# Kernel tuning notes

Measured on AMD Instinct MI355X. Metric: run time of the kernel, lower is better.

The kernel has to match this reference:

```python
import jax, jax.numpy as jnp
import numpy as np

D_MODEL = 1024
D_FFN = 4096
NUM_EXPERTS = 8
TOP_K = 2
EPS = 1e-7


def setup_inputs() -> dict:
    key = jax.random.key(0)
    ks = jax.random.split(key, 10)
    B, T = 2, 2048
    s = 0.02
    return {
        "x": jax.random.normal(ks[0], (B, T, D_MODEL), dtype=jnp.float32),
        "padding_mask": jnp.ones((B, T), dtype=bool),
        "rms_w": jnp.ones((D_MODEL,), dtype=jnp.float32),
        "router_w": jax.random.normal(ks[1], (NUM_EXPERTS, D_MODEL), dtype=jnp.float32) * s,
        "router_b": jnp.zeros((NUM_EXPERTS,), dtype=jnp.float32),
        "W1": jax.random.normal(ks[2], (NUM_EXPERTS, D_MODEL, D_FFN), dtype=jnp.float32) * s,
        "b1": jnp.zeros((NUM_EXPERTS, D_FFN), dtype=jnp.float32),
        "W2": jax.random.normal(ks[3], (NUM_EXPERTS, D_FFN, D_MODEL), dtype=jnp.float32) * s,
        "b2": jnp.zeros((NUM_EXPERTS, D_MODEL), dtype=jnp.float32),
        "W3": jax.random.normal(ks[4], (NUM_EXPERTS, D_MODEL, D_FFN), dtype=jnp.float32) * s,
        "b3": jnp.zeros((NUM_EXPERTS, D_FFN), dtype=jnp.float32),
    }


def reference(x, padding_mask, rms_w, router_w, router_b, W1, b1, W2, b2, W3, b3):
    B, T, d = x.shape
    # RMSNorm
    rms = jnp.sqrt(jnp.mean(x * x, axis=-1, keepdims=True) + EPS)
    xn = rms_w * (x / rms)
    xf = xn.reshape(-1, d)  # [N, d]

    # Router: softmax -> top-k -> renormalize
    logits = xf @ router_w.T + router_b            # [N, E]
    probs = jax.nn.softmax(logits, axis=-1)
    topv, topi = jax.lax.top_k(probs, TOP_K)       # [N, K]
    w = topv / jnp.sum(topv, axis=-1, keepdims=True)
    # Dense combine weights per (token, expert): sum of top-k weights routed to e
    combine = jnp.sum(jax.nn.one_hot(topi, NUM_EXPERTS, dtype=xf.dtype) * w[..., None], axis=1)  # [N, E]

    # Loop over experts via scan (one full-token SwiGLU FFN per expert, masked combine)
    def step(acc, params):
        W1e, b1e, W2e, b2e, W3e, b3e, ce = params
        h = jax.nn.silu(xf @ W1e + b1e) * (xf @ W3e + b3e)  # [N, d_ffn]
        y = h @ W2e + b2e                                    # [N, d]
        return acc + ce[:, None] * y, None

    out, _ = jax.lax.scan(step, jnp.zeros_like(xf), (W1, b1, W2, b2, W3, b3, combine.T))
    aux_loss = jnp.asarray(0.0, dtype=x.dtype)  # use_aux_loss only active in training mode
    return out.reshape(B, T, d), aux_loss
```

## Files before the change

### kernel.cpp

```cpp
#include <hip/hip_runtime.h>
#include <stdint.h>


#define NTOK 4096
#define DM   1024
#define DF   4096
#define NE   8
#define BM   128
#define MAX_RB 72
#define SLOT_CAP (MAX_RB * BM)

typedef _Float16 f16;
typedef __attribute__((ext_vector_type(8))) _Float16 f16x8;
typedef __attribute__((ext_vector_type(4))) _Float16 f16x4;
typedef __attribute__((ext_vector_type(4))) float    f32x4;
typedef __attribute__((ext_vector_type(2))) float    f32x2;

__device__ __forceinline__ void gl2lds16(const void* g, void* l) {
  __builtin_amdgcn_global_load_lds(
      (const __attribute__((address_space(1))) unsigned int*)g,
      (__attribute__((address_space(3))) unsigned int*)l, 16, 0, 0);
}

__global__ __launch_bounds__(256) void k_rms_router(
    const float* __restrict__ x, const float* __restrict__ rms_w,
    const float* __restrict__ rw, const float* __restrict__ rbias,
    f16* __restrict__ xn, int* __restrict__ topi, float* __restrict__ topw,
    int* __restrict__ counts)
{
  int t = blockIdx.x;
  int tid = threadIdx.x;
  const float* xr = x + (size_t)t * DM;
  f32x4 xv = *(const f32x4*)(xr + tid * 4);
  f32x4 gw = *(const f32x4*)(rms_w + tid * 4);
  f32x4 gv = xv * gw;

  float v[9];
  v[8] = xv[0]*xv[0] + xv[1]*xv[1] + xv[2]*xv[2] + xv[3]*xv[3];
#pragma unroll
  for (int e = 0; e < NE; ++e) {
    f32x4 wv = *(const f32x4*)(rw + e * DM + tid * 4);
    v[e] = gv[0]*wv[0] + gv[1]*wv[1] + gv[2]*wv[2] + gv[3]*wv[3];
  }
#pragma unroll
  for (int off = 32; off; off >>= 1) {
#pragma unroll
    for (int j = 0; j < 9; ++j) v[j] += __shfl_xor(v[j], off);
  }
  __shared__ float red[4][9];
  int wave = tid >> 6, lane = tid & 63;
  if (lane == 0) {
#pragma unroll
    for (int j = 0; j < 9; ++j) red[wave][j] = v[j];
  }
  __syncthreads();
  float tot[9];
#pragma unroll
  for (int j = 0; j < 9; ++j)
    tot[j] = red[0][j] + red[1][j] + red[2][j] + red[3][j];

  float rinv = 1.0f / sqrtf(tot[8] * (1.0f / DM) + 1e-7f);
  float lg[NE];
#pragma unroll
  for (int e = 0; e < NE; ++e) lg[e] = tot[e] * rinv + rbias[e];

  int e1 = 0; float b1v = lg[0];
#pragma unroll
  for (int e = 1; e < NE; ++e) if (lg[e] > b1v) { b1v = lg[e]; e1 = e; }
  int e2 = -1; float b2v = -1e30f;
#pragma unroll
  for (int e = 0; e < NE; ++e) if (e != e1 && lg[e] > b2v) { b2v = lg[e]; e2 = e; }

  float r2 = expf(b2v - b1v);
  float w1 = 1.0f / (1.0f + r2);
  float w2 = r2 * w1;

  if (tid == 0) {
    topi[t * 2 + 0] = e1; topi[t * 2 + 1] = e2;
    topw[t * 2 + 0] = w1; topw[t * 2 + 1] = w2;
    atomicAdd(&counts[e1], 1);
    atomicAdd(&counts[e2], 1);
  }
  f16x4 o;
#pragma unroll
  for (int i = 0; i < 4; ++i) o[i] = (f16)(gv[i] * rinv);
  *(f16x4*)(xn + (size_t)t * DM + tid * 4) = o;
}

__global__ void k_build(const int* __restrict__ counts, int* __restrict__ po,
                        int2* __restrict__ rbtable, int* __restrict__ total_rb)
{
  if (threadIdx.x != 0 || blockIdx.x != 0) return;
  int off = 0, idx = 0;
  for (int e = 0; e < NE; ++e) {
    int c = counts[e];
    po[e] = off;
    int nrb = (c + BM - 1) / BM;
    for (int r = 0; r < nrb; ++r) { rbtable[idx] = make_int2(e, off + r * BM); ++idx; }
    off += nrb * BM;
  }
  *total_rb = idx;
}

__global__ __launch_bounds__(256) void k_assign(
    const int* __restrict__ topi, const float* __restrict__ topw,
    const int* __restrict__ po, int* __restrict__ cursors,
    int* __restrict__ slot_token, float* __restrict__ slot_w)
{
  int t = blockIdx.x * 256 + threadIdx.x;
  if (t >= NTOK) return;
#pragma unroll
  for (int k = 0; k < 2; ++k) {
    int e = topi[t * 2 + k];
    int pos = atomicAdd(&cursors[e], 1);
    int slot = po[e] + pos;
    slot_token[slot] = t;
    slot_w[slot] = topw[t * 2 + k];
  }
}

__global__ __launch_bounds__(256) void k_convw(
    const float* __restrict__ W1, const float* __restrict__ W3,
    const float* __restrict__ W2, f16* __restrict__ w16)
{
  __shared__ f16 T[64][132];
  int g = blockIdx.x;
  int tensor = g >> 12;
  int rem = g & 4095;
  int e = rem >> 9;
  int t = rem & 511;
  const float* W; int nstride, np, kt;
  if (tensor == 2) { W = W2; nstride = DM; np = t >> 6; kt = t & 63; }
  else { W = (tensor == 0) ? W1 : W3; nstride = DF; np = t >> 4; kt = t & 15; }
  const float* src = W + (size_t)e * DM * DF + (size_t)(kt * 64) * nstride + np * 128;

  int tid = threadIdx.x;
  int q = tid & 31, kb = tid >> 5;
#pragma unroll
  for (int i = 0; i < 8; ++i) {
    int k = kb + 8 * i;
    f32x4 v = *(const f32x4*)(src + (size_t)k * nstride + q * 4);
    f16x4 h4 = { (f16)v[0], (f16)v[1], (f16)v[2], (f16)v[3] };
    *(f16x4*)(&T[k][q * 4]) = h4;
  }
  __syncthreads();
  int n = tid >> 1;
  f16* dst = w16 + ((size_t)(tensor * NE + e) * 512 + t) * 8192 + n * 64 + (tid & 1) * 32;
#pragma unroll
  for (int qq = 0; qq < 4; ++qq) {
    int cs = (tid & 1) * 4 + qq;
    int cl = cs ^ (n & 7);
    f16x8 o;
#pragma unroll
    for (int j = 0; j < 8; ++j) o[j] = T[cl * 8 + j][n];
    *(f16x8*)(dst + qq * 8) = o;
  }
}

__global__ __launch_bounds__(256, 2) void k_ffn13(
    const f16* __restrict__ xn, const int* __restrict__ slot_token,
    const int2* __restrict__ rbtable, const int* __restrict__ total_rb,
    const f16* __restrict__ w16,
    const float* __restrict__ b1, const float* __restrict__ b3,
    f16* __restrict__ h)
{
  int bid = blockIdx.x;
  int wl = (bid & 7) * 288 + (bid >> 3);
  int rbi = wl % 72;
  int np  = wl / 72;
  if (rbi >= *total_rb) return;
  int2 ent = rbtable[rbi];
  int e = ent.x, row0 = ent.y;
  int n0 = np * 128;

  __shared__ __align__(16) f16 As[128 * 64];
  __shared__ __align__(16) f16 Bs[2][128 * 64];

  int tid = threadIdx.x, lane = tid & 63, wave = tid >> 6;
  int wm = wave >> 1, wn = wave & 1;

  const f16* wb1 = w16 + ((size_t)(0 * NE + e) * 512 + np * 16) * 8192;
  const f16* wb3 = w16 + ((size_t)(1 * NE + e) * 512 + np * 16) * 8192;

  int tok[4];
#pragma unroll
  for (int q = 0; q < 4; ++q) {
    int m = q * 32 + wave * 8 + (lane >> 3);
    int tkn = slot_token[row0 + m];
    tok[q] = (tkn < 0) ? 0 : tkn;
  }
  int csx = (((lane & 7) ^ (lane >> 3)) << 3);
  int lin = wave * 512 + lane * 8;

  f32x4 acc1[4][4], acc3[4][4];
  f32x4 z = {0.f, 0.f, 0.f, 0.f};
#pragma unroll
  for (int i = 0; i < 4; ++i)
#pragma unroll
    for (int j = 0; j < 4; ++j) { acc1[i][j] = z; acc3[i][j] = z; }

  for (int kt = 0; kt < DM / 64; ++kt) {
    int k0 = kt * 64;
    const f16* s1 = wb1 + (size_t)kt * 8192;
    const f16* s3 = wb3 + (size_t)kt * 8192;
#pragma unroll
    for (int q = 0; q < 4; ++q) {
      gl2lds16(xn + (size_t)tok[q] * DM + k0 + csx,
               (char*)As + q * 4096 + wave * 1024);
      gl2lds16(s1 + q * 2048 + lin, (char*)Bs[0] + q * 4096 + wave * 1024);
      gl2lds16(s3 + q * 2048 + lin, (char*)Bs[1] + q * 4096 + wave * 1024);
    }
    __syncthreads();
#pragma unroll
    for (int kh = 0; kh < 2; ++kh) {
      int kk = kh * 32 + (lane >> 4) * 8;
      f16x8 a[4];
#pragma unroll
      for (int fm = 0; fm < 4; ++fm) {
        int m = wm * 64 + fm * 16 + (lane & 15);
        a[fm] = *(const f16x8*)((char*)As + m * 128 + 2 * (kk ^ ((m & 7) << 3)));
      }
#pragma unroll
      for (int fn = 0; fn < 4; ++fn) {
        int n = wn * 64 + fn * 16 + (lane & 15);
        f16x8 bf1 = *(const f16x8*)((char*)Bs[0] + n * 128 + 2 * (kk ^ ((n & 7) << 3)));
        f16x8 bf3 = *(const f16x8*)((char*)Bs[1] + n * 128 + 2 * (kk ^ ((n & 7) << 3)));
#pragma unroll
        for (int fm = 0; fm < 4; ++fm) {
          acc1[fm][fn] = __builtin_amdgcn_mfma_f32_16x16x32_f16(a[fm], bf1, acc1[fm][fn], 0, 0, 0);
          acc3[fm][fn] = __builtin_amdgcn_mfma_f32_16x16x32_f16(a[fm], bf3, acc3[fm][fn], 0, 0, 0);
        }
      }
    }
    __syncthreads();
  }
#pragma unroll
  for (int fn = 0; fn < 4; ++fn) {
    int nc = n0 + wn * 64 + fn * 16 + (lane & 15);
    float bb1 = b1[e * DF + nc], bb3 = b3[e * DF + nc];
#pragma unroll
    for (int fm = 0; fm < 4; ++fm) {
      int mbase = wm * 64 + fm * 16 + (lane >> 4) * 4;
#pragma unroll
      for (int r = 0; r < 4; ++r) {
        int sl = mbase + r;
        float u1 = acc1[fm][fn][r] + bb1;
        float u3 = acc3[fm][fn][r] + bb3;
        float hv = (u1 / (1.0f + __expf(-u1))) * u3;
        size_t off = (size_t)(row0 + sl) * DF + (nc & ~63)
                   + ((((nc >> 3) & 7) ^ (sl & 7)) << 3) + (nc & 7);
        h[off] = (f16)hv;
      }
    }
  }
}

__global__ __launch_bounds__(256, 2) void k_ffn2(
    const f16* __restrict__ h, const int* __restrict__ slot_token,
    const float* __restrict__ slot_w,
    const int2* __restrict__ rbtable, const int* __restrict__ total_rb,
    const f16* __restrict__ w16, const float* __restrict__ b2,
    float* __restrict__ out)
{
  int bid = blockIdx.x;
  int wl = (bid & 7) * 72 + (bid >> 3);
  int rbi = wl % 72;
  int np  = wl / 72;
  if (rbi >= *total_rb) return;
  int2 ent = rbtable[rbi];
  int e = ent.x, row0 = ent.y;
  int n0 = np * 128;

  __shared__ __align__(16) f16 As[128 * 64];
  __shared__ __align__(16) f16 Bsh[128 * 64];

  int tid = threadIdx.x, lane = tid & 63, wave = tid >> 6;
  int wm = wave >> 1, wn = wave & 1;
  const f16* wb = w16 + ((size_t)(2 * NE + e) * 512 + np * 64) * 8192;
  int lin = wave * 512 + lane * 8;

  f32x4 acc[4][4];
  f32x4 z = {0.f, 0.f, 0.f, 0.f};
#pragma unroll
  for (int i = 0; i < 4; ++i)
#pragma unroll
    for (int j = 0; j < 4; ++j) acc[i][j] = z;

  for (int kt = 0; kt < DF / 64; ++kt) {
    const f16* sB = wb + (size_t)kt * 8192;
#pragma unroll
    for (int q = 0; q < 4; ++q) {
      int m = q * 32 + wave * 8 + (lane >> 3);
      gl2lds16(h + (size_t)(row0 + m) * DF + kt * 64 + ((lane & 7) << 3),
               (char*)As + q * 4096 + wave * 1024);
      gl2lds16(sB + q * 2048 + lin, (char*)Bsh + q * 4096 + wave * 1024);
    }
    __syncthreads();
#pragma unroll
    for (int kh = 0; kh < 2; ++kh) {
      int kk = kh * 32 + (lane >> 4) * 8;
      f16x8 a[4];
#pragma unroll
      for (int fm = 0; fm < 4; ++fm) {
        int m = wm * 64 + fm * 16 + (lane & 15);
        a[fm] = *(const f16x8*)((char*)As + m * 128 + 2 * (kk ^ ((m & 7) << 3)));
      }
#pragma unroll
      for (int fn = 0; fn < 4; ++fn) {
        int n = wn * 64 + fn * 16 + (lane & 15);
        f16x8 bf = *(const f16x8*)((char*)Bsh + n * 128 + 2 * (kk ^ ((n & 7) << 3)));
#pragma unroll
        for (int fm = 0; fm < 4; ++fm)
          acc[fm][fn] = __builtin_amdgcn_mfma_f32_16x16x32_f16(a[fm], bf, acc[fm][fn], 0, 0, 0);
      }
    }
    __syncthreads();
  }
  int   tk[4][4];
  float cw[4][4];
#pragma unroll
  for (int fm = 0; fm < 4; ++fm) {
#pragma unroll
    for (int r = 0; r < 4; ++r) {
      int slot = row0 + wm * 64 + fm * 16 + (lane >> 4) * 4 + r;
      tk[fm][r] = slot_token[slot];
      cw[fm][r] = slot_w[slot];
    }
  }
#pragma unroll
  for (int fn = 0; fn < 4; ++fn) {
    int nc = n0 + wn * 64 + fn * 16 + (lane & 15);
    float bb = b2[e * DM + nc];
#pragma unroll
    for (int fm = 0; fm < 4; ++fm) {
#pragma unroll
      for (int r = 0; r < 4; ++r) {
        if (tk[fm][r] >= 0)
          atomicAdd(out + (size_t)tk[fm][r] * DM + nc, cw[fm][r] * (acc[fm][fn][r] + bb));
      }
    }
  }
}

extern "C" void kernel_launch(void* const* d_in, const int* in_sizes, int n_in,
                              void* d_out, int out_size, void* d_ws, size_t ws_size,
                              hipStream_t stream)
{
  const float* x     = (const float*)d_in[0];
  const float* rms_w = (const float*)d_in[2];
  const float* rw    = (const float*)d_in[3];
  const float* rbias = (const float*)d_in[4];
  const float* W1    = (const float*)d_in[5];
  const float* b1    = (const float*)d_in[6];
  const float* W2    = (const float*)d_in[7];
  const float* b2    = (const float*)d_in[8];
  const float* W3    = (const float*)d_in[9];
  const float* b3    = (const float*)d_in[10];
  float* out = (float*)d_out;

  char* ws = (char*)d_ws;
  size_t o = 0;
  f16* w16 = (f16*)(ws + o); o += (size_t)3 * NE * 512 * 8192 * 2;
  f16* h   = (f16*)(ws + o); o += (size_t)SLOT_CAP * DF * 2;
  f16* xn  = (f16*)(ws + o); o += (size_t)NTOK * DM * 2;
  int*   slot_token = (int*)(ws + o);   o += SLOT_CAP * 4;
  float* slot_w     = (float*)(ws + o); o += SLOT_CAP * 4;
  int*   topi       = (int*)(ws + o);   o += NTOK * 2 * 4;
  float* topw       = (float*)(ws + o); o += NTOK * 2 * 4;
  int*   counts     = (int*)(ws + o);   o += 64;
  int*   cursors    = (int*)(ws + o);   o += 64;
  int*   po         = (int*)(ws + o);   o += 64;
  int*   total_rb   = (int*)(ws + o);   o += 64;
  int2*  rbtable    = (int2*)(ws + o);  o += MAX_RB * 8;
  (void)ws_size; (void)in_sizes; (void)n_in;

  hipMemsetAsync(d_out, 0, (size_t)out_size * 4, stream);
  hipMemsetAsync(counts, 0, 128, stream);
  hipMemsetAsync(slot_token, 0xFF, SLOT_CAP * 4, stream);

  k_convw<<<3 * NE * 512, 256, 0, stream>>>(W1, W3, W2, w16);
  k_rms_router<<<NTOK, 256, 0, stream>>>(x, rms_w, rw, rbias, xn, topi, topw, counts);
  k_build<<<1, 64, 0, stream>>>(counts, po, rbtable, total_rb);
  k_assign<<<16, 256, 0, stream>>>(topi, topw, po, cursors, slot_token, slot_w);
  k_ffn13<<<8 * 288, 256, 0, stream>>>(xn, slot_token, rbtable, total_rb,
                                       w16, b1, b3, h);
  k_ffn2<<<8 * 72, 256, 0, stream>>>(h, slot_token, slot_w, rbtable, total_rb,
                                     w16, b2, out);
}
```

Baseline: 579.1 us.

## Double-buffer LDS tiles and use eight waves in both FFN GEMM kernels

Both expert GEMM kernels now keep two LDS buffers. The next K-tile is loaded asynchronously straight from global to LDS while the current tile runs on the MFMA units, so each iteration drops one barrier-bounded load phase. Blocks grow from 256 to 512 threads, and each wave now computes a 32x64 sub-tile instead of 64x64. That lowers accumulator registers per wave and raises the number of waves in flight. In exchange the first kernel's LDS use rises to 96KB per block, which may limit it to one resident block per CU, and each wave does less MFMA work per LDS read.

```diff
diff --git a/kernel.cpp b/kernel.cpp
--- a/kernel.cpp
+++ b/kernel.cpp
@@ -157,7 +157,7 @@
   }
 }
 
-__global__ __launch_bounds__(256, 2) void k_ffn13(
+__global__ __launch_bounds__(512, 2) void k_ffn13(
     const f16* __restrict__ xn, const int* __restrict__ slot_token,
     const int2* __restrict__ rbtable, const int* __restrict__ total_rb,
     const f16* __restrict__ w16,
@@ -173,8 +173,8 @@
   int e = ent.x, row0 = ent.y;
   int n0 = np * 128;
 
-  __shared__ __align__(16) f16 As[128 * 64];
-  __shared__ __align__(16) f16 Bs[2][128 * 64];
+  __shared__ __align__(16) f16 As[2][8192];
+  __shared__ __align__(16) f16 Bs[2][2][8192];
 
   int tid = threadIdx.x, lane = tid & 63, wave = tid >> 6;
   int wm = wave >> 1, wn = wave & 1;
@@ -182,51 +182,57 @@
   const f16* wb1 = w16 + ((size_t)(0 * NE + e) * 512 + np * 16) * 8192;
   const f16* wb3 = w16 + ((size_t)(1 * NE + e) * 512 + np * 16) * 8192;
 
-  int tok[4];
-#pragma unroll
-  for (int q = 0; q < 4; ++q) {
-    int m = q * 32 + wave * 8 + (lane >> 3);
+  int tok[2];
+#pragma unroll
+  for (int q = 0; q < 2; ++q) {
+    int m = q * 64 + wave * 8 + (lane >> 3);
     int tkn = slot_token[row0 + m];
     tok[q] = (tkn < 0) ? 0 : tkn;
   }
   int csx = (((lane & 7) ^ (lane >> 3)) << 3);
   int lin = wave * 512 + lane * 8;
 
-  f32x4 acc1[4][4], acc3[4][4];
+  f32x4 acc1[2][4], acc3[2][4];
   f32x4 z = {0.f, 0.f, 0.f, 0.f};
 #pragma unroll
-  for (int i = 0; i < 4; ++i)
+  for (int i = 0; i < 2; ++i)
 #pragma unroll
     for (int j = 0; j < 4; ++j) { acc1[i][j] = z; acc3[i][j] = z; }
 
-  for (int kt = 0; kt < DM / 64; ++kt) {
-    int k0 = kt * 64;
+  auto STAGE = [&](int kt, int bf) {
     const f16* s1 = wb1 + (size_t)kt * 8192;
     const f16* s3 = wb3 + (size_t)kt * 8192;
-#pragma unroll
-    for (int q = 0; q < 4; ++q) {
+    int k0 = kt * 64;
+#pragma unroll
+    for (int q = 0; q < 2; ++q) {
       gl2lds16(xn + (size_t)tok[q] * DM + k0 + csx,
-               (char*)As + q * 4096 + wave * 1024);
-      gl2lds16(s1 + q * 2048 + lin, (char*)Bs[0] + q * 4096 + wave * 1024);
-      gl2lds16(s3 + q * 2048 + lin, (char*)Bs[1] + q * 4096 + wave * 1024);
-    }
-    __syncthreads();
+               (char*)As[bf] + q * 8192 + wave * 1024);
+      gl2lds16(s1 + q * 4096 + lin, (char*)Bs[bf][0] + q * 8192 + wave * 1024);
+      gl2lds16(s3 + q * 4096 + lin, (char*)Bs[bf][1] + q * 8192 + wave * 1024);
+    }
+  };
+
+  STAGE(0, 0);
+  __syncthreads();
+  for (int kt = 0; kt < DM / 64; ++kt) {
+    int cur = kt & 1;
+    if (kt < DM / 64 - 1) STAGE(kt + 1, cur ^ 1);
 #pragma unroll
     for (int kh = 0; kh < 2; ++kh) {
       int kk = kh * 32 + (lane >> 4) * 8;
-      f16x8 a[4];
-#pragma unroll
-      for (int fm = 0; fm < 4; ++fm) {
-        int m = wm * 64 + fm * 16 + (lane & 15);
-        a[fm] = *(const f16x8*)((char*)As + m * 128 + 2 * (kk ^ ((m & 7) << 3)));
+      f16x8 a[2];
+#pragma unroll
+      for (int fm = 0; fm < 2; ++fm) {
+        int m = wm * 32 + fm * 16 + (lane & 15);
+        a[fm] = *(const f16x8*)((char*)As[cur] + m * 128 + 2 * (kk ^ ((m & 7) << 3)));
       }
 #pragma unroll
       for (int fn = 0; fn < 4; ++fn) {
         int n = wn * 64 + fn * 16 + (lane & 15);
-        f16x8 bf1 = *(const f16x8*)((char*)Bs[0] + n * 128 + 2 * (kk ^ ((n & 7) << 3)));
-        f16x8 bf3 = *(const f16x8*)((char*)Bs[1] + n * 128 + 2 * (kk ^ ((n & 7) << 3)));
-#pragma unroll
-        for (int fm = 0; fm < 4; ++fm) {
+        f16x8 bf1 = *(const f16x8*)((char*)Bs[cur][0] + n * 128 + 2 * (kk ^ ((n & 7) << 3)));
+        f16x8 bf3 = *(const f16x8*)((char*)Bs[cur][1] + n * 128 + 2 * (kk ^ ((n & 7) << 3)));
+#pragma unroll
+        for (int fm = 0; fm < 2; ++fm) {
           acc1[fm][fn] = __builtin_amdgcn_mfma_f32_16x16x32_f16(a[fm], bf1, acc1[fm][fn], 0, 0, 0);
           acc3[fm][fn] = __builtin_amdgcn_mfma_f32_16x16x32_f16(a[fm], bf3, acc3[fm][fn], 0, 0, 0);
         }
@@ -239,8 +245,8 @@
     int nc = n0 + wn * 64 + fn * 16 + (lane & 15);
     float bb1 = b1[e * DF + nc], bb3 = b3[e * DF + nc];
 #pragma unroll
-    for (int fm = 0; fm < 4; ++fm) {
-      int mbase = wm * 64 + fm * 16 + (lane >> 4) * 4;
+    for (int fm = 0; fm < 2; ++fm) {
+      int mbase = wm * 32 + fm * 16 + (lane >> 4) * 4;
 #pragma unroll
       for (int r = 0; r < 4; ++r) {
         int sl = mbase + r;
@@ -255,7 +261,7 @@
   }
 }
 
-__global__ __launch_bounds__(256, 2) void k_ffn2(
+__global__ __launch_bounds__(512, 4) void k_ffn2(
     const f16* __restrict__ h, const int* __restrict__ slot_token,
     const float* __restrict__ slot_w,
     const int2* __restrict__ rbtable, const int* __restrict__ total_rb,
@@ -271,58 +277,64 @@
   int e = ent.x, row0 = ent.y;
   int n0 = np * 128;
 
-  __shared__ __align__(16) f16 As[128 * 64];
-  __shared__ __align__(16) f16 Bsh[128 * 64];
+  __shared__ __align__(16) f16 As[2][8192];
+  __shared__ __align__(16) f16 Bsh[2][8192];
 
   int tid = threadIdx.x, lane = tid & 63, wave = tid >> 6;
   int wm = wave >> 1, wn = wave & 1;
   const f16* wb = w16 + ((size_t)(2 * NE + e) * 512 + np * 64) * 8192;
   int lin = wave * 512 + lane * 8;
 
-  f32x4 acc[4][4];
+  f32x4 acc[2][4];
   f32x4 z = {0.f, 0.f, 0.f, 0.f};
 #pragma unroll
-  for (int i = 0; i < 4; ++i)
+  for (int i = 0; i < 2; ++i)
 #pragma unroll
     for (int j = 0; j < 4; ++j) acc[i][j] = z;
 
+  auto STAGE = [&](int kt, int bf) {
+    const f16* sB = wb + (size_t)kt * 8192;
+#pragma unroll
+    for (int q = 0; q < 2; ++q) {
+      int m = q * 64 + wave * 8 + (lane >> 3);
+      gl2lds16(h + (size_t)(row0 + m) * DF + kt * 64 + ((lane & 7) << 3),
+               (char*)As[bf] + q * 8192 + wave * 1024);
+      gl2lds16(sB + q * 4096 + lin, (char*)Bsh[bf] + q * 8192 + wave * 1024);
+    }
+  };
+
+  STAGE(0, 0);
+  __syncthreads();
   for (int kt = 0; kt < DF / 64; ++kt) {
-    const f16* sB = wb + (size_t)kt * 8192;
-#pragma unroll
-    for (int q = 0; q < 4; ++q) {
-      int m = q * 32 + wave * 8 + (lane >> 3);
-      gl2lds16(h + (size_t)(row0 + m) * DF + kt * 64 + ((lane & 7) << 3),
-               (char*)As + q * 4096 + wave * 1024);
-      gl2lds16(sB + q * 2048 + lin, (char*)Bsh + q * 4096 + wave * 1024);
-    }
-    __syncthreads();
+    int cur = kt & 1;
+    if (kt < DF / 64 - 1) STAGE(kt + 1, cur ^ 1);
 #pragma unroll
     for (int kh = 0; kh < 2; ++kh) {
       int kk = kh * 32 + (lane >> 4) * 8;
-      f16x8 a[4];
-#pragma unroll
-      for (int fm = 0; fm < 4; ++fm) {
-        int m = wm * 64 + fm * 16 + (lane & 15);
-        a[fm] = *(const f16x8*)((char*)As + m * 128 + 2 * (kk ^ ((m & 7) << 3)));
+      f16x8 a[2];
+#pragma unroll
+      for (int fm = 0; fm < 2; ++fm) {
+        int m = wm * 32 + fm * 16 + (lane & 15);
+        a[fm] = *(const f16x8*)((char*)As[cur] + m * 128 + 2 * (kk ^ ((m & 7) << 3)));
       }
 #pragma unroll
       for (int fn = 0; fn < 4; ++fn) {
         int n = wn * 64 + fn * 16 + (lane & 15);
-        f16x8 bf = *(const f16x8*)((char*)Bsh + n * 128 + 2 * (kk ^ ((n & 7) << 3)));
-#pragma unroll
-        for (int fm = 0; fm < 4; ++fm)
+        f16x8 bf = *(const f16x8*)((char*)Bsh[cur] + n * 128 + 2 * (kk ^ ((n & 7) << 3)));
+#pragma unroll
+        for (int fm = 0; fm < 2; ++fm)
           acc[fm][fn] = __builtin_amdgcn_mfma_f32_16x16x32_f16(a[fm], bf, acc[fm][fn], 0, 0, 0);
       }
     }
     __syncthreads();
   }
-  int   tk[4][4];
-  float cw[4][4];
-#pragma unroll
-  for (int fm = 0; fm < 4; ++fm) {
+  int   tk[2][4];
+  float cw[2][4];
+#pragma unroll
+  for (int fm = 0; fm < 2; ++fm) {
 #pragma unroll
     for (int r = 0; r < 4; ++r) {
-      int slot = row0 + wm * 64 + fm * 16 + (lane >> 4) * 4 + r;
+      int slot = row0 + wm * 32 + fm * 16 + (lane >> 4) * 4 + r;
       tk[fm][r] = slot_token[slot];
       cw[fm][r] = slot_w[slot];
     }
@@ -332,7 +344,7 @@
     int nc = n0 + wn * 64 + fn * 16 + (lane & 15);
     float bb = b2[e * DM + nc];
 #pragma unroll
-    for (int fm = 0; fm < 4; ++fm) {
+    for (int fm = 0; fm < 2; ++fm) {
 #pragma unroll
       for (int r = 0; r < 4; ++r) {
         if (tk[fm][r] >= 0)
@@ -382,8 +394,8 @@
   k_rms_router<<<NTOK, 256, 0, stream>>>(x, rms_w, rw, rbias, xn, topi, topw, counts);
   k_build<<<1, 64, 0, stream>>>(counts, po, rbtable, total_rb);
   k_assign<<<16, 256, 0, stream>>>(topi, topw, po, cursors, slot_token, slot_w);
-  k_ffn13<<<8 * 288, 256, 0, stream>>>(xn, slot_token, rbtable, total_rb,
+  k_ffn13<<<8 * 288, 512, 0, stream>>>(xn, slot_token, rbtable, total_rb,
                                        w16, b1, b3, h);
-  k_ffn2<<<8 * 72, 256, 0, stream>>>(h, slot_token, slot_w, rbtable, total_rb,
+  k_ffn2<<<8 * 72, 512, 0, stream>>>(h, slot_token, slot_w, rbtable, total_rb,
                                      w16, b2, out);
 }
```

Measured after the change: 692.9 us. +19.7%, slower.
